# Kernel optimization log

Measured on AMD Instinct MI355X. Metric: run time of the kernel, lower is better.

Reference implementation:

```python
import jax, jax.numpy as jnp
import numpy as np

B, M, S, E, LC, V, HOPS = 16, 2048, 6, 128, 512, 32000, 3
PAD = 1


def setup_inputs() -> dict:
    key = jax.random.key(0)
    ks = jax.random.split(key, 16)
    story = jax.random.randint(ks[0], (B, M, S), 0, V)
    kb_len = jax.random.randint(ks[1], (B,), 0, M - LC)
    conv_len = jax.random.randint(ks[2], (B,), 0, LC)
    hidden = jax.random.normal(ks[3], (1, B, 2 * E), jnp.float32)
    dh_outputs = jax.random.normal(ks[4], (B, LC, E), jnp.float32)
    tf_hidden = jax.random.normal(ks[5], (B, E), jnp.float32)
    query_vector = jax.random.normal(ks[6], (B, E), jnp.float32)
    global_pointer = jax.random.uniform(ks[7], (B, M), jnp.float32)
    C = jax.random.normal(ks[8], (HOPS + 1, V, E), jnp.float32) * 0.1
    C = C.at[:, PAD, :].set(0.0)  # padding_idx row is zero
    s = 0.05
    wA1 = jax.random.normal(ks[9], (2 * E, E), jnp.float32) * s
    bA1 = jnp.zeros((E,), jnp.float32)
    wA2 = jax.random.normal(ks[10], (E, E), jnp.float32) * s
    bA2 = jnp.zeros((E,), jnp.float32)
    wC1 = jax.random.normal(ks[11], (2 * E, E), jnp.float32) * s
    bC1 = jnp.zeros((E,), jnp.float32)
    wC2 = jax.random.normal(ks[12], (E, E), jnp.float32) * s
    bC2 = jnp.zeros((E,), jnp.float32)
    wf = jax.random.normal(ks[13], (2 * E, E), jnp.float32) * s
    bf = jnp.zeros((E,), jnp.float32)
    return dict(story=story, kb_len=kb_len, conv_len=conv_len, hidden=hidden,
                dh_outputs=dh_outputs, tf_hidden=tf_hidden, query_vector=query_vector,
                global_pointer=global_pointer, C=C, wA1=wA1, bA1=bA1, wA2=wA2, bA2=bA2,
                wC1=wC1, bC1=bC1, wC2=wC2, bC2=bC2, wf=wf, bf=bf)


def _lrelu(x):
    return jnp.where(x > 0, x, 0.1 * x)  # LeakyReLU(0.1)


def _mlp(x, w1, b1, w2, b2):
    return _lrelu(x @ w1 + b1) @ w2 + b2


def _add_lm(mem, kb_len, conv_len, dh):
    # mem: [B,M,E]; add dh[bi,:conv_len[bi]] into rows [kb_len, kb_len+conv_len)
    pos = jnp.arange(mem.shape[1])[None, :]            # [1,M]
    idx = pos - kb_len[:, None]                        # [B,M]
    mask = (idx >= 0) & (idx < conv_len[:, None])
    gathered = jnp.take_along_axis(dh, jnp.clip(idx, 0, dh.shape[1] - 1)[..., None], axis=1)
    return mem + jnp.where(mask[..., None], gathered, 0.0)


def reference(story, kb_len, conv_len, hidden, dh_outputs, tf_hidden,
              query_vector, global_pointer, C, wA1, bA1, wA2, bA2,
              wC1, bC1, wC2, bC2, wf, bf):
    # --- load_ent_memory: build m_story_ent (dropout off / eval mode) ---
    u = _lrelu(hidden[0] @ wf + bf)                    # hidden.squeeze(0) -> [B,E]
    tf = jnp.broadcast_to(tf_hidden[:, None, :], (B, M, E))
    m_story = []
    eC = None
    for hop in range(HOPS):
        eA = _add_lm(C[hop][story].sum(2), kb_len, conv_len, dh_outputs)       # [B,M,E]
        eA = _mlp(jnp.concatenate([eA, tf], -1), wA1, bA1, wA2, bA2)
        logit = jnp.einsum('bme,be->bm', eA, u)
        p = jax.nn.softmax(logit, axis=1)
        eC = _add_lm(C[hop + 1][story].sum(2), kb_len, conv_len, dh_outputs)   # [B,M,E]
        eC = _mlp(jnp.concatenate([eC, tf], -1), wC1, bC1, wC2, bC2)
        u = u + jnp.einsum('bme,bm->be', eC, p)
        m_story.append(eA)
    m_story.append(eC)
    # --- forward(query_vector, global_pointer) ---
    uq = query_vector
    gp = global_pointer[..., None]                     # [B,M,1]
    prob_logits = None
    prob_soft = None
    for hop in range(HOPS):
        mA = m_story[hop] * gp
        prob_logits = jnp.einsum('bme,be->bm', mA, uq)
        prob_soft = jax.nn.softmax(prob_logits, axis=1)
        mC = m_story[hop + 1] * gp
        uq = uq + jnp.einsum('bme,bm->be', mC, prob_soft)
    return (prob_soft, prob_logits)
```

## Files before the change

kernel.cpp:

```cpp
#include <hip/hip_runtime.h>
#include <math.h>

#define BB 16
#define MM 2048
#define SS 6
#define EE 128
#define LCC 512
#define VV 32000

typedef __attribute__((ext_vector_type(8))) __bf16 bf16x8;
typedef __attribute__((ext_vector_type(4))) float f32x4;

#define XS_STRIDE 264
#define HS_STRIDE 136

static __device__ inline void cvt8(const float* __restrict__ src, __bf16* __restrict__ dst) {
    const float4 a = *(const float4*)src;
    const float4 b = *(const float4*)(src + 4);
    bf16x8 o;
    o[0] = (__bf16)a.x; o[1] = (__bf16)a.y; o[2] = (__bf16)a.z; o[3] = (__bf16)a.w;
    o[4] = (__bf16)b.x; o[5] = (__bf16)b.y; o[6] = (__bf16)b.z; o[7] = (__bf16)b.w;
    *(bf16x8*)dst = o;
}

#define N_C8  (3 * VV * EE / 8)
#define N_D8  (BB * LCC * EE / 8)
#define N_T8  (BB * EE / 8)
#define N_W1  (256 * 128)
#define N_W2  (128 * 128)
#define N_UQ  (BB * EE)
#define N_PREP (N_C8 + N_D8 + N_T8 + N_W1 + N_W2 + N_UQ)

__global__ __launch_bounds__(256)
void megaprep(const float* __restrict__ C, const float* __restrict__ dh,
              const float* __restrict__ tf, const float* __restrict__ W1,
              const float* __restrict__ W2, const float* __restrict__ query,
              __bf16* __restrict__ Cb, __bf16* __restrict__ dhb,
              __bf16* __restrict__ tfb, __bf16* __restrict__ w1t,
              __bf16* __restrict__ w2t, float* __restrict__ uqA,
              float* __restrict__ uqB)
{
    int i = blockIdx.x * 256 + threadIdx.x;
    if (i < N_C8) { cvt8(C + (size_t)i * 8, Cb + (size_t)i * 8); return; }
    i -= N_C8;
    if (i < N_D8) { cvt8(dh + (size_t)i * 8, dhb + (size_t)i * 8); return; }
    i -= N_D8;
    if (i < N_T8) { cvt8(tf + i * 8, tfb + i * 8); return; }
    i -= N_T8;
    if (i < N_W1) { const int n = i >> 8, k = i & 255; w1t[i] = (__bf16)W1[k * EE + n]; return; }
    i -= N_W1;
    if (i < N_W2) { const int n = i >> 7, k = i & 127; w2t[i] = (__bf16)W2[k * EE + n]; return; }
    i -= N_W2;
    if (i < N_UQ) { uqA[i] = query[i]; uqB[i] = 0.f; }
}

__global__ __launch_bounds__(256)
void embed_mlp_mfma(const int* __restrict__ story,
                    const int* __restrict__ kb_len,
                    const int* __restrict__ conv_len,
                    const __bf16* __restrict__ Cb,
                    const __bf16* __restrict__ dhb,
                    const __bf16* __restrict__ tfb,
                    const __bf16* __restrict__ w1t, const float* __restrict__ b1,
                    const __bf16* __restrict__ w2t, const float* __restrict__ b2,
                    const float* __restrict__ gp, const float* __restrict__ query,
                    __bf16* __restrict__ mout, float* __restrict__ lbuf0)
{
    __shared__ __bf16 Xs[32 * XS_STRIDE];
    __shared__ __bf16 Hs[32 * HS_STRIDE];
    __shared__ int    sidx[32 * SS];
    float* plog = (float*)Hs;

    const int bid  = blockIdx.x;
    const int hop  = bid >> 10;
    const int row0 = (bid & 1023) * 32;
    const int b    = row0 >> 11;
    const int tid  = threadIdx.x;

    const __bf16* Ck = Cb + (size_t)hop * VV * EE;

    for (int i = tid; i < 32 * SS; i += 256) sidx[i] = story[(size_t)row0 * SS + i];

    const int kb   = kb_len[b];
    const int cl   = conv_len[b];
    const int rgrp = tid >> 4;
    const int e8   = (tid & 15) * 8;
    const bf16x8 tf8 = *(const bf16x8*)&tfb[b * EE + e8];
    __syncthreads();

    bf16x8 g[2][SS], dv[2];
    #pragma unroll
    for (int p = 0; p < 2; ++p) {
        const int r = p * 16 + rgrp;
        const int* si = &sidx[r * SS];
        #pragma unroll
        for (int s = 0; s < SS; ++s)
            g[p][s] = *(const bf16x8*)&Ck[(size_t)si[s] * EE + e8];
        const int j = ((row0 + r) & (MM - 1)) - kb;
        if (j >= 0 && j < cl) {
            dv[p] = *(const bf16x8*)&dhb[((size_t)b * LCC + j) * EE + e8];
        } else {
            bf16x8 z;
            #pragma unroll
            for (int q = 0; q < 8; ++q) z[q] = (__bf16)0.f;
            dv[p] = z;
        }
    }
    #pragma unroll
    for (int p = 0; p < 2; ++p) {
        const int r = p * 16 + rgrp;
        bf16x8 pk;
        #pragma unroll
        for (int q = 0; q < 8; ++q) {
            float s = (float)dv[p][q];
            #pragma unroll
            for (int s6 = 0; s6 < SS; ++s6) s += (float)g[p][s6][q];
            pk[q] = (__bf16)s;
        }
        *(bf16x8*)&Xs[r * XS_STRIDE + e8]      = pk;
        *(bf16x8*)&Xs[r * XS_STRIDE + EE + e8] = tf8;
    }
    __syncthreads();

    const int w       = tid >> 6;
    const int lane    = tid & 63;
    const int lr      = lane & 15;
    const int lk      = lane >> 4;
    const int colbase = w * 32;

    f32x4 acc1[2][2];
    #pragma unroll
    for (int i = 0; i < 2; ++i)
        #pragma unroll
        for (int j = 0; j < 2; ++j) acc1[i][j] = (f32x4){0.f, 0.f, 0.f, 0.f};

    for (int ks = 0; ks < 8; ++ks) {
        bf16x8 a[2], bw[2];
        #pragma unroll
        for (int mt = 0; mt < 2; ++mt)
            a[mt] = *(const bf16x8*)&Xs[(mt * 16 + lr) * XS_STRIDE + ks * 32 + lk * 8];
        #pragma unroll
        for (int nt = 0; nt < 2; ++nt)
            bw[nt] = *(const bf16x8*)&w1t[(size_t)(colbase + nt * 16 + lr) * 256 + ks * 32 + lk * 8];
        #pragma unroll
        for (int mt = 0; mt < 2; ++mt)
            #pragma unroll
            for (int nt = 0; nt < 2; ++nt)
                acc1[mt][nt] = __builtin_amdgcn_mfma_f32_16x16x32_bf16(a[mt], bw[nt], acc1[mt][nt], 0, 0, 0);
    }
    {
        const float b1v[2] = { b1[colbase + lr], b1[colbase + 16 + lr] };
        #pragma unroll
        for (int mt = 0; mt < 2; ++mt)
            #pragma unroll
            for (int nt = 0; nt < 2; ++nt)
                #pragma unroll
                for (int reg = 0; reg < 4; ++reg) {
                    float h = acc1[mt][nt][reg] + b1v[nt];
                    h = (h > 0.f) ? h : 0.1f * h;
                    Hs[(mt * 16 + lk * 4 + reg) * HS_STRIDE + colbase + nt * 16 + lr] = (__bf16)h;
                }
    }
    __syncthreads();

    f32x4 acc2[2][2];
    #pragma unroll
    for (int i = 0; i < 2; ++i)
        #pragma unroll
        for (int j = 0; j < 2; ++j) acc2[i][j] = (f32x4){0.f, 0.f, 0.f, 0.f};

    for (int ks = 0; ks < 4; ++ks) {
        bf16x8 a[2], bw[2];
        #pragma unroll
        for (int mt = 0; mt < 2; ++mt)
            a[mt] = *(const bf16x8*)&Hs[(mt * 16 + lr) * HS_STRIDE + ks * 32 + lk * 8];
        #pragma unroll
        for (int nt = 0; nt < 2; ++nt)
            bw[nt] = *(const bf16x8*)&w2t[(size_t)(colbase + nt * 16 + lr) * 128 + ks * 32 + lk * 8];
        #pragma unroll
        for (int mt = 0; mt < 2; ++mt)
            #pragma unroll
            for (int nt = 0; nt < 2; ++nt)
                acc2[mt][nt] = __builtin_amdgcn_mfma_f32_16x16x32_bf16(a[mt], bw[nt], acc2[mt][nt], 0, 0, 0);
    }

    const float b2v[2] = { b2[colbase + lr], b2[colbase + 16 + lr] };

    if (hop == 0) {
        const float qv0 = query[b * EE + colbase + lr];
        const float qv1 = query[b * EE + colbase + 16 + lr];
        __syncthreads();
        #pragma unroll
        for (int mt = 0; mt < 2; ++mt)
            #pragma unroll
            for (int reg = 0; reg < 4; ++reg) {
                float p = (acc2[mt][0][reg] + b2v[0]) * qv0
                        + (acc2[mt][1][reg] + b2v[1]) * qv1;
                p += __shfl_xor(p, 1, 64);
                p += __shfl_xor(p, 2, 64);
                p += __shfl_xor(p, 4, 64);
                p += __shfl_xor(p, 8, 64);
                if (lr == 0) plog[(mt * 16 + lk * 4 + reg) * 4 + w] = p;
            }
        __syncthreads();
        if (tid < 32) {
            const float l = plog[tid * 4] + plog[tid * 4 + 1] + plog[tid * 4 + 2] + plog[tid * 4 + 3];
            lbuf0[row0 + tid] = l * gp[row0 + tid];
        }
    } else {
        __bf16* out = mout + (size_t)(hop - 1) * 32768 * EE;
        #pragma unroll
        for (int mt = 0; mt < 2; ++mt)
            #pragma unroll
            for (int nt = 0; nt < 2; ++nt)
                #pragma unroll
                for (int reg = 0; reg < 4; ++reg) {
                    const int rg_ = row0 + mt * 16 + lk * 4 + reg;
                    out[(size_t)rg_ * EE + colbase + nt * 16 + lr] =
                        (__bf16)(acc2[mt][nt][reg] + b2v[nt]);
                }
    }
}

__global__ __launch_bounds__(256)
void update_kernel(const __bf16* __restrict__ mk, const float* __restrict__ gp,
                   const float* __restrict__ lbuf, float* __restrict__ uq)
{
    __shared__ float redm[4], reds[4];
    __shared__ float wls[64];
    __shared__ float part[4][128];

    const int b      = blockIdx.x >> 5;
    const int rloc0  = (blockIdx.x & 31) * 64;
    const int tid    = threadIdx.x;
    const int lane   = tid & 63;
    const int w      = tid >> 6;
    const float* lb  = lbuf + (size_t)b * MM;

    float v[8];
    float mx = -1e30f;
    #pragma unroll
    for (int i = 0; i < 8; ++i) { v[i] = lb[i * 256 + tid]; mx = fmaxf(mx, v[i]); }
    #pragma unroll
    for (int off = 32; off > 0; off >>= 1) mx = fmaxf(mx, __shfl_xor(mx, off, 64));
    if (lane == 0) redm[w] = mx;
    __syncthreads();
    mx = fmaxf(fmaxf(redm[0], redm[1]), fmaxf(redm[2], redm[3]));
    float sum = 0.f;
    #pragma unroll
    for (int i = 0; i < 8; ++i) sum += __expf(v[i] - mx);
    #pragma unroll
    for (int off = 32; off > 0; off >>= 1) sum += __shfl_xor(sum, off, 64);
    if (lane == 0) reds[w] = sum;
    __syncthreads();
    const float inv = 1.f / (reds[0] + reds[1] + reds[2] + reds[3]);

    if (tid < 64)
        wls[tid] = gp[(size_t)b * MM + rloc0 + tid] * __expf(lb[rloc0 + tid] - mx) * inv;
    __syncthreads();

    const int rgrp = tid >> 4;
    const int e8   = (tid & 15) * 8;
    float acc[8];
    #pragma unroll
    for (int q = 0; q < 8; ++q) acc[q] = 0.f;
    #pragma unroll
    for (int p = 0; p < 4; ++p) {
        const int rl  = p * 16 + rgrp;
        const float wg = wls[rl];
        const bf16x8 vv = *(const bf16x8*)&mk[((size_t)b * MM + rloc0 + rl) * EE + e8];
        #pragma unroll
        for (int q = 0; q < 8; ++q) acc[q] += wg * (float)vv[q];
    }
    #pragma unroll
    for (int q = 0; q < 8; ++q) {
        acc[q] += __shfl_xor(acc[q], 16, 64);
        acc[q] += __shfl_xor(acc[q], 32, 64);
    }
    if (lane < 16) {
        #pragma unroll
        for (int q = 0; q < 8; ++q) part[w][e8 + q] = acc[q];
    }
    __syncthreads();
    if (tid < 128) {
        const float s = part[0][tid] + part[1][tid] + part[2][tid] + part[3][tid];
        atomicAdd(&uq[b * EE + tid], s);
    }
}

__global__ __launch_bounds__(256)
void logits_kernel(const __bf16* __restrict__ mk, const float* __restrict__ gp,
                   const float* __restrict__ uqa, const float* __restrict__ uqb,
                   float* __restrict__ out)
{
    __shared__ float uqs[128];
    const int row0 = blockIdx.x * 64;
    const int b    = row0 >> 11;
    const int tid  = threadIdx.x;
    if (tid < 128) uqs[tid] = uqa[b * EE + tid] + (uqb ? uqb[b * EE + tid] : 0.f);
    __syncthreads();
    const int w = tid >> 6, lane = tid & 63;
    const int g = lane >> 4, l16 = lane & 15;
    float u[8];
    #pragma unroll
    for (int j = 0; j < 8; ++j) u[j] = uqs[l16 * 8 + j];
    #pragma unroll
    for (int it = 0; it < 4; ++it) {
        const int row = row0 + it * 16 + w * 4 + g;
        const bf16x8 v = *(const bf16x8*)&mk[(size_t)row * EE + l16 * 8];
        float p = 0.f;
        #pragma unroll
        for (int j = 0; j < 8; ++j) p += (float)v[j] * u[j];
        p += __shfl_xor(p, 1, 64);
        p += __shfl_xor(p, 2, 64);
        p += __shfl_xor(p, 4, 64);
        p += __shfl_xor(p, 8, 64);
        if (l16 == 0) out[row] = p * gp[row];
    }
}

__global__ __launch_bounds__(256)
void softmax_final(const float* __restrict__ logits, float* __restrict__ soft)
{
    __shared__ float redm[4], reds[4];
    const int b = blockIdx.x, tid = threadIdx.x;
    const int lane = tid & 63, w = tid >> 6;
    const float* lb = logits + (size_t)b * MM;
    float v[8];
    float mx = -1e30f;
    #pragma unroll
    for (int i = 0; i < 8; ++i) { v[i] = lb[i * 256 + tid]; mx = fmaxf(mx, v[i]); }
    #pragma unroll
    for (int off = 32; off > 0; off >>= 1) mx = fmaxf(mx, __shfl_xor(mx, off, 64));
    if (lane == 0) redm[w] = mx;
    __syncthreads();
    mx = fmaxf(fmaxf(redm[0], redm[1]), fmaxf(redm[2], redm[3]));
    float sum = 0.f;
    #pragma unroll
    for (int i = 0; i < 8; ++i) { v[i] = __expf(v[i] - mx); sum += v[i]; }
    #pragma unroll
    for (int off = 32; off > 0; off >>= 1) sum += __shfl_xor(sum, off, 64);
    if (lane == 0) reds[w] = sum;
    __syncthreads();
    const float inv = 1.f / (reds[0] + reds[1] + reds[2] + reds[3]);
    #pragma unroll
    for (int i = 0; i < 8; ++i) soft[(size_t)b * MM + i * 256 + tid] = v[i] * inv;
}

extern "C" void kernel_launch(void* const* d_in, const int* in_sizes, int n_in,
                              void* d_out, int out_size, void* d_ws, size_t ws_size,
                              hipStream_t stream) {
    const int*   story    = (const int*)d_in[0];
    const int*   kb_len   = (const int*)d_in[1];
    const int*   conv_len = (const int*)d_in[2];
    const float* dh       = (const float*)d_in[4];
    const float* tf       = (const float*)d_in[5];
    const float* query    = (const float*)d_in[6];
    const float* gp       = (const float*)d_in[7];
    const float* C        = (const float*)d_in[8];
    const float* wA1      = (const float*)d_in[9];
    const float* bA1      = (const float*)d_in[10];
    const float* wA2      = (const float*)d_in[11];
    const float* bA2      = (const float*)d_in[12];

    char* ws = (char*)d_ws;
    const size_t M_ELEMS = (size_t)32768 * EE;
    size_t off = 0;
    __bf16* m   = (__bf16*)(ws + off); off += 2 * M_ELEMS * sizeof(__bf16);
    __bf16* Cb  = (__bf16*)(ws + off); off += (size_t)3 * VV * EE * sizeof(__bf16);
    __bf16* dhb = (__bf16*)(ws + off); off += (size_t)BB * LCC * EE * sizeof(__bf16);
    __bf16* tfb = (__bf16*)(ws + off); off += (size_t)BB * EE * sizeof(__bf16);
    __bf16* w1t = (__bf16*)(ws + off); off += 256 * 128 * sizeof(__bf16);
    __bf16* w2t = (__bf16*)(ws + off); off += 128 * 128 * sizeof(__bf16);
    float* lbuf = (float*)(ws + off);  off += (size_t)BB * MM * sizeof(float);
    float* uqA  = (float*)(ws + off);  off += (size_t)BB * EE * sizeof(float);
    float* uqB  = (float*)(ws + off);  off += (size_t)BB * EE * sizeof(float);

    float* out_soft   = (float*)d_out;
    float* out_logits = out_soft + (size_t)BB * MM;

    megaprep<<<N_PREP / 256, 256, 0, stream>>>(C, dh, tf, wA1, wA2, query,
                                               Cb, dhb, tfb, w1t, w2t, uqA, uqB);
    embed_mlp_mfma<<<3072, 256, 0, stream>>>(story, kb_len, conv_len, Cb, dhb, tfb,
                                             w1t, bA1, w2t, bA2, gp, query, m, lbuf);
    update_kernel<<<512, 256, 0, stream>>>(m, gp, lbuf, uqA);
    logits_kernel<<<512, 256, 0, stream>>>(m, gp, uqA, nullptr, lbuf);
    update_kernel<<<512, 256, 0, stream>>>(m + M_ELEMS, gp, lbuf, uqB);
    logits_kernel<<<512, 256, 0, stream>>>(m + M_ELEMS, gp, uqA, uqB, out_logits);
    softmax_final<<<BB, 256, 0, stream>>>(out_logits, out_soft);
}
```

Baseline: 195.1 us.

## Fuse hop update, logits and softmax into one per-batch tail kernel

Replaces the five tail launches (two update, two logits, one softmax) with a single kernel that runs one 1024-thread block per batch and loops over the hops, keeping uq and the logits in shared memory. This removes the atomics, the uq initialisation in the prep kernel and several launch gaps. The trade-off is that only 16 blocks run the tail, so most CUs sit idle while each block streams 2 MB of bf16 per hop. Separately, the embed kernel now reuses the Xs shared buffer for Hs, with an extra barrier before Hs is written, and declares launch bounds of 8 blocks per CU to raise occupancy.

```diff
diff --git a/kernel.cpp b/kernel.cpp
--- a/kernel.cpp
+++ b/kernel.cpp
@@ -28,17 +28,15 @@
 #define N_T8  (BB * EE / 8)
 #define N_W1  (256 * 128)
 #define N_W2  (128 * 128)
-#define N_UQ  (BB * EE)
-#define N_PREP (N_C8 + N_D8 + N_T8 + N_W1 + N_W2 + N_UQ)
+#define N_PREP (N_C8 + N_D8 + N_T8 + N_W1 + N_W2)
 
 __global__ __launch_bounds__(256)
 void megaprep(const float* __restrict__ C, const float* __restrict__ dh,
               const float* __restrict__ tf, const float* __restrict__ W1,
-              const float* __restrict__ W2, const float* __restrict__ query,
+              const float* __restrict__ W2,
               __bf16* __restrict__ Cb, __bf16* __restrict__ dhb,
               __bf16* __restrict__ tfb, __bf16* __restrict__ w1t,
-              __bf16* __restrict__ w2t, float* __restrict__ uqA,
-              float* __restrict__ uqB)
+              __bf16* __restrict__ w2t)
 {
     int i = blockIdx.x * 256 + threadIdx.x;
     if (i < N_C8) { cvt8(C + (size_t)i * 8, Cb + (size_t)i * 8); return; }
@@ -49,12 +47,10 @@
     i -= N_T8;
     if (i < N_W1) { const int n = i >> 8, k = i & 255; w1t[i] = (__bf16)W1[k * EE + n]; return; }
     i -= N_W1;
-    if (i < N_W2) { const int n = i >> 7, k = i & 127; w2t[i] = (__bf16)W2[k * EE + n]; return; }
-    i -= N_W2;
-    if (i < N_UQ) { uqA[i] = query[i]; uqB[i] = 0.f; }
-}
-
-__global__ __launch_bounds__(256)
+    if (i < N_W2) { const int n = i >> 7, k = i & 127; w2t[i] = (__bf16)W2[k * EE + n]; }
+}
+
+__global__ __launch_bounds__(256, 8)
 void embed_mlp_mfma(const int* __restrict__ story,
                     const int* __restrict__ kb_len,
                     const int* __restrict__ conv_len,
@@ -67,9 +63,9 @@
                     __bf16* __restrict__ mout, float* __restrict__ lbuf0)
 {
     __shared__ __bf16 Xs[32 * XS_STRIDE];
-    __shared__ __bf16 Hs[32 * HS_STRIDE];
     __shared__ int    sidx[32 * SS];
-    float* plog = (float*)Hs;
+    __bf16* Hs   = Xs;
+    float*  plog = (float*)Xs;
 
     const int bid  = blockIdx.x;
     const int hop  = bid >> 10;
@@ -148,6 +144,7 @@
             for (int nt = 0; nt < 2; ++nt)
                 acc1[mt][nt] = __builtin_amdgcn_mfma_f32_16x16x32_bf16(a[mt], bw[nt], acc1[mt][nt], 0, 0, 0);
     }
+    __syncthreads();
     {
         const float b1v[2] = { b1[colbase + lr], b1[colbase + 16 + lr] };
         #pragma unroll
@@ -222,129 +219,111 @@
     }
 }
 
-__global__ __launch_bounds__(256)
-void update_kernel(const __bf16* __restrict__ mk, const float* __restrict__ gp,
-                   const float* __restrict__ lbuf, float* __restrict__ uq)
-{
-    __shared__ float redm[4], reds[4];
-    __shared__ float wls[64];
-    __shared__ float part[4][128];
-
-    const int b      = blockIdx.x >> 5;
-    const int rloc0  = (blockIdx.x & 31) * 64;
-    const int tid    = threadIdx.x;
-    const int lane   = tid & 63;
-    const int w      = tid >> 6;
-    const float* lb  = lbuf + (size_t)b * MM;
-
-    float v[8];
-    float mx = -1e30f;
-    #pragma unroll
-    for (int i = 0; i < 8; ++i) { v[i] = lb[i * 256 + tid]; mx = fmaxf(mx, v[i]); }
-    #pragma unroll
-    for (int off = 32; off > 0; off >>= 1) mx = fmaxf(mx, __shfl_xor(mx, off, 64));
-    if (lane == 0) redm[w] = mx;
-    __syncthreads();
-    mx = fmaxf(fmaxf(redm[0], redm[1]), fmaxf(redm[2], redm[3]));
-    float sum = 0.f;
-    #pragma unroll
-    for (int i = 0; i < 8; ++i) sum += __expf(v[i] - mx);
-    #pragma unroll
-    for (int off = 32; off > 0; off >>= 1) sum += __shfl_xor(sum, off, 64);
-    if (lane == 0) reds[w] = sum;
-    __syncthreads();
-    const float inv = 1.f / (reds[0] + reds[1] + reds[2] + reds[3]);
-
-    if (tid < 64)
-        wls[tid] = gp[(size_t)b * MM + rloc0 + tid] * __expf(lb[rloc0 + tid] - mx) * inv;
-    __syncthreads();
-
-    const int rgrp = tid >> 4;
-    const int e8   = (tid & 15) * 8;
-    float acc[8];
-    #pragma unroll
-    for (int q = 0; q < 8; ++q) acc[q] = 0.f;
-    #pragma unroll
-    for (int p = 0; p < 4; ++p) {
-        const int rl  = p * 16 + rgrp;
-        const float wg = wls[rl];
-        const bf16x8 vv = *(const bf16x8*)&mk[((size_t)b * MM + rloc0 + rl) * EE + e8];
-        #pragma unroll
-        for (int q = 0; q < 8; ++q) acc[q] += wg * (float)vv[q];
-    }
-    #pragma unroll
-    for (int q = 0; q < 8; ++q) {
-        acc[q] += __shfl_xor(acc[q], 16, 64);
-        acc[q] += __shfl_xor(acc[q], 32, 64);
-    }
-    if (lane < 16) {
-        #pragma unroll
-        for (int q = 0; q < 8; ++q) part[w][e8 + q] = acc[q];
-    }
-    __syncthreads();
-    if (tid < 128) {
-        const float s = part[0][tid] + part[1][tid] + part[2][tid] + part[3][tid];
-        atomicAdd(&uq[b * EE + tid], s);
-    }
-}
-
-__global__ __launch_bounds__(256)
-void logits_kernel(const __bf16* __restrict__ mk, const float* __restrict__ gp,
-                   const float* __restrict__ uqa, const float* __restrict__ uqb,
-                   float* __restrict__ out)
+__global__ __launch_bounds__(1024)
+void tail_kernel(const __bf16* __restrict__ m, const float* __restrict__ gp,
+                 const float* __restrict__ lbuf0, const float* __restrict__ query,
+                 float* __restrict__ out_logits, float* __restrict__ out_soft)
 {
     __shared__ float uqs[128];
-    const int row0 = blockIdx.x * 64;
-    const int b    = row0 >> 11;
+    __shared__ float wls[2048];
+    __shared__ float lls[2048];
+    __shared__ float part[16][128];
+    __shared__ float redm[16], reds[16];
+
+    const int b    = blockIdx.x;
     const int tid  = threadIdx.x;
-    if (tid < 128) uqs[tid] = uqa[b * EE + tid] + (uqb ? uqb[b * EE + tid] : 0.f);
-    __syncthreads();
-    const int w = tid >> 6, lane = tid & 63;
-    const int g = lane >> 4, l16 = lane & 15;
-    float u[8];
-    #pragma unroll
-    for (int j = 0; j < 8; ++j) u[j] = uqs[l16 * 8 + j];
-    #pragma unroll
-    for (int it = 0; it < 4; ++it) {
-        const int row = row0 + it * 16 + w * 4 + g;
-        const bf16x8 v = *(const bf16x8*)&mk[(size_t)row * EE + l16 * 8];
-        float p = 0.f;
-        #pragma unroll
-        for (int j = 0; j < 8; ++j) p += (float)v[j] * u[j];
-        p += __shfl_xor(p, 1, 64);
-        p += __shfl_xor(p, 2, 64);
-        p += __shfl_xor(p, 4, 64);
-        p += __shfl_xor(p, 8, 64);
-        if (l16 == 0) out[row] = p * gp[row];
-    }
-}
-
-__global__ __launch_bounds__(256)
-void softmax_final(const float* __restrict__ logits, float* __restrict__ soft)
-{
-    __shared__ float redm[4], reds[4];
-    const int b = blockIdx.x, tid = threadIdx.x;
-    const int lane = tid & 63, w = tid >> 6;
-    const float* lb = logits + (size_t)b * MM;
-    float v[8];
-    float mx = -1e30f;
-    #pragma unroll
-    for (int i = 0; i < 8; ++i) { v[i] = lb[i * 256 + tid]; mx = fmaxf(mx, v[i]); }
-    #pragma unroll
-    for (int off = 32; off > 0; off >>= 1) mx = fmaxf(mx, __shfl_xor(mx, off, 64));
-    if (lane == 0) redm[w] = mx;
-    __syncthreads();
-    mx = fmaxf(fmaxf(redm[0], redm[1]), fmaxf(redm[2], redm[3]));
-    float sum = 0.f;
-    #pragma unroll
-    for (int i = 0; i < 8; ++i) { v[i] = __expf(v[i] - mx); sum += v[i]; }
-    #pragma unroll
-    for (int off = 32; off > 0; off >>= 1) sum += __shfl_xor(sum, off, 64);
-    if (lane == 0) reds[w] = sum;
-    __syncthreads();
-    const float inv = 1.f / (reds[0] + reds[1] + reds[2] + reds[3]);
-    #pragma unroll
-    for (int i = 0; i < 8; ++i) soft[(size_t)b * MM + i * 256 + tid] = v[i] * inv;
+    const int w    = tid >> 6;
+    const int lane = tid & 63;
+    const int g    = lane >> 4;
+    const int l16  = lane & 15;
+    const float* gpb = gp + (size_t)b * MM;
+
+    if (tid < 128) uqs[tid] = query[b * EE + tid];
+    lls[tid]        = lbuf0[(size_t)b * MM + tid];
+    lls[tid + 1024] = lbuf0[(size_t)b * MM + tid + 1024];
+    __syncthreads();
+
+    for (int hop = 0; hop < 3; ++hop) {
+        const float v0 = lls[tid], v1 = lls[tid + 1024];
+        float mx = fmaxf(v0, v1);
+        #pragma unroll
+        for (int off = 32; off > 0; off >>= 1) mx = fmaxf(mx, __shfl_xor(mx, off, 64));
+        if (lane == 0) redm[w] = mx;
+        __syncthreads();
+        float bmx = redm[0];
+        #pragma unroll
+        for (int i = 1; i < 16; ++i) bmx = fmaxf(bmx, redm[i]);
+        const float e0 = __expf(v0 - bmx), e1 = __expf(v1 - bmx);
+        float sm = e0 + e1;
+        #pragma unroll
+        for (int off = 32; off > 0; off >>= 1) sm += __shfl_xor(sm, off, 64);
+        if (lane == 0) reds[w] = sm;
+        __syncthreads();
+        float bs = 0.f;
+        #pragma unroll
+        for (int i = 0; i < 16; ++i) bs += reds[i];
+        const float inv = 1.f / bs;
+
+        if (hop == 2) {
+            out_soft[(size_t)b * MM + tid]        = e0 * inv;
+            out_soft[(size_t)b * MM + tid + 1024] = e1 * inv;
+            return;
+        }
+        wls[tid]        = e0 * inv * gpb[tid];
+        wls[tid + 1024] = e1 * inv * gpb[tid + 1024];
+        __syncthreads();
+
+        const __bf16* mh = m + ((size_t)hop * 32768 + (size_t)b * MM) * EE;
+
+        float acc[8];
+        #pragma unroll
+        for (int q = 0; q < 8; ++q) acc[q] = 0.f;
+        for (int it = 0; it < 32; ++it) {
+            const int row = w * 128 + it * 4 + g;
+            const bf16x8 mv = *(const bf16x8*)&mh[(size_t)row * EE + l16 * 8];
+            const float wg = wls[row];
+            #pragma unroll
+            for (int q = 0; q < 8; ++q) acc[q] += wg * (float)mv[q];
+        }
+        #pragma unroll
+        for (int q = 0; q < 8; ++q) {
+            acc[q] += __shfl_xor(acc[q], 16, 64);
+            acc[q] += __shfl_xor(acc[q], 32, 64);
+        }
+        if (lane < 16) {
+            #pragma unroll
+            for (int q = 0; q < 8; ++q) part[w][l16 * 8 + q] = acc[q];
+        }
+        __syncthreads();
+        if (tid < 128) {
+            float s = uqs[tid];
+            #pragma unroll
+            for (int ww = 0; ww < 16; ++ww) s += part[ww][tid];
+            uqs[tid] = s;
+        }
+        __syncthreads();
+
+        float u[8];
+        #pragma unroll
+        for (int j = 0; j < 8; ++j) u[j] = uqs[l16 * 8 + j];
+        for (int it = 0; it < 32; ++it) {
+            const int row = w * 128 + it * 4 + g;
+            const bf16x8 mv = *(const bf16x8*)&mh[(size_t)row * EE + l16 * 8];
+            float p = 0.f;
+            #pragma unroll
+            for (int j = 0; j < 8; ++j) p += (float)mv[j] * u[j];
+            p += __shfl_xor(p, 1, 64);
+            p += __shfl_xor(p, 2, 64);
+            p += __shfl_xor(p, 4, 64);
+            p += __shfl_xor(p, 8, 64);
+            if (l16 == 0) {
+                const float lv = p * gpb[row];
+                lls[row] = lv;
+                if (hop == 1) out_logits[(size_t)b * MM + row] = lv;
+            }
+        }
+        __syncthreads();
+    }
 }
 
 extern "C" void kernel_launch(void* const* d_in, const int* in_sizes, int n_in,
@@ -373,19 +352,13 @@
     __bf16* w1t = (__bf16*)(ws + off); off += 256 * 128 * sizeof(__bf16);
     __bf16* w2t = (__bf16*)(ws + off); off += 128 * 128 * sizeof(__bf16);
     float* lbuf = (float*)(ws + off);  off += (size_t)BB * MM * sizeof(float);
-    float* uqA  = (float*)(ws + off);  off += (size_t)BB * EE * sizeof(float);
-    float* uqB  = (float*)(ws + off);  off += (size_t)BB * EE * sizeof(float);
 
     float* out_soft   = (float*)d_out;
     float* out_logits = out_soft + (size_t)BB * MM;
 
-    megaprep<<<N_PREP / 256, 256, 0, stream>>>(C, dh, tf, wA1, wA2, query,
-                                               Cb, dhb, tfb, w1t, w2t, uqA, uqB);
+    megaprep<<<N_PREP / 256, 256, 0, stream>>>(C, dh, tf, wA1, wA2,
+                                               Cb, dhb, tfb, w1t, w2t);
     embed_mlp_mfma<<<3072, 256, 0, stream>>>(story, kb_len, conv_len, Cb, dhb, tfb,
                                              w1t, bA1, w2t, bA2, gp, query, m, lbuf);
-    update_kernel<<<512, 256, 0, stream>>>(m, gp, lbuf, uqA);
-    logits_kernel<<<512, 256, 0, stream>>>(m, gp, uqA, nullptr, lbuf);
-    update_kernel<<<512, 256, 0, stream>>>(m + M_ELEMS, gp, lbuf, uqB);
-    logits_kernel<<<512, 256, 0, stream>>>(m + M_ELEMS, gp, uqA, uqB, out_logits);
-    softmax_final<<<BB, 256, 0, stream>>>(out_logits, out_soft);
-}
+    tail_kernel<<<BB, 1024, 0, stream>>>(m, gp, lbuf, query, out_logits, out_soft);
+}
```

Measured after the change: 239.2 us. 22.6% more time.

## Gather fp32 embeddings directly instead of pre-converting the whole table to bf16

Applied to the files above, without the earlier changes.

Removes the prep pass that converted the full embedding tables, dialogue outputs and tf vector to bf16. The embed kernel now gathers fp32 rows, sums them in fp32 and packs to bf16 in shared memory. The query term is folded into the logits kernel instead of being copied into the accumulator. This trades a large streaming conversion pass for twice the bytes per gathered row.

```diff
diff --git a/kernel.cpp b/kernel.cpp
--- a/kernel.cpp
+++ b/kernel.cpp
@@ -14,53 +14,38 @@
 #define XS_STRIDE 264
 #define HS_STRIDE 136
 
-static __device__ inline void cvt8(const float* __restrict__ src, __bf16* __restrict__ dst) {
-    const float4 a = *(const float4*)src;
-    const float4 b = *(const float4*)(src + 4);
-    bf16x8 o;
-    o[0] = (__bf16)a.x; o[1] = (__bf16)a.y; o[2] = (__bf16)a.z; o[3] = (__bf16)a.w;
-    o[4] = (__bf16)b.x; o[5] = (__bf16)b.y; o[6] = (__bf16)b.z; o[7] = (__bf16)b.w;
-    *(bf16x8*)dst = o;
-}
-
-#define N_C8  (3 * VV * EE / 8)
-#define N_D8  (BB * LCC * EE / 8)
-#define N_T8  (BB * EE / 8)
+static __device__ inline unsigned short bfbits(float x) {
+    __bf16 h = (__bf16)x;
+    return __builtin_bit_cast(unsigned short, h);
+}
+
 #define N_W1  (256 * 128)
 #define N_W2  (128 * 128)
 #define N_UQ  (BB * EE)
-#define N_PREP (N_C8 + N_D8 + N_T8 + N_W1 + N_W2 + N_UQ)
-
-__global__ __launch_bounds__(256)
-void megaprep(const float* __restrict__ C, const float* __restrict__ dh,
-              const float* __restrict__ tf, const float* __restrict__ W1,
-              const float* __restrict__ W2, const float* __restrict__ query,
-              __bf16* __restrict__ Cb, __bf16* __restrict__ dhb,
-              __bf16* __restrict__ tfb, __bf16* __restrict__ w1t,
-              __bf16* __restrict__ w2t, float* __restrict__ uqA,
-              float* __restrict__ uqB)
+#define N_PREP (N_W1 + N_W2 + 2 * N_UQ)
+
+__global__ __launch_bounds__(256)
+void prep_small(const float* __restrict__ W1, const float* __restrict__ W2,
+                __bf16* __restrict__ w1t, __bf16* __restrict__ w2t,
+                float* __restrict__ uqA, float* __restrict__ uqB)
 {
     int i = blockIdx.x * 256 + threadIdx.x;
-    if (i < N_C8) { cvt8(C + (size_t)i * 8, Cb + (size_t)i * 8); return; }
-    i -= N_C8;
-    if (i < N_D8) { cvt8(dh + (size_t)i * 8, dhb + (size_t)i * 8); return; }
-    i -= N_D8;
-    if (i < N_T8) { cvt8(tf + i * 8, tfb + i * 8); return; }
-    i -= N_T8;
     if (i < N_W1) { const int n = i >> 8, k = i & 255; w1t[i] = (__bf16)W1[k * EE + n]; return; }
     i -= N_W1;
     if (i < N_W2) { const int n = i >> 7, k = i & 127; w2t[i] = (__bf16)W2[k * EE + n]; return; }
     i -= N_W2;
-    if (i < N_UQ) { uqA[i] = query[i]; uqB[i] = 0.f; }
+    if (i < N_UQ) { uqA[i] = 0.f; return; }
+    i -= N_UQ;
+    if (i < N_UQ) { uqB[i] = 0.f; }
 }
 
 __global__ __launch_bounds__(256)
 void embed_mlp_mfma(const int* __restrict__ story,
                     const int* __restrict__ kb_len,
                     const int* __restrict__ conv_len,
-                    const __bf16* __restrict__ Cb,
-                    const __bf16* __restrict__ dhb,
-                    const __bf16* __restrict__ tfb,
+                    const float* __restrict__ dh,
+                    const float* __restrict__ tf,
+                    const float* __restrict__ C,
                     const __bf16* __restrict__ w1t, const float* __restrict__ b1,
                     const __bf16* __restrict__ w2t, const float* __restrict__ b2,
                     const float* __restrict__ gp, const float* __restrict__ query,
@@ -77,48 +62,38 @@
     const int b    = row0 >> 11;
     const int tid  = threadIdx.x;
 
-    const __bf16* Ck = Cb + (size_t)hop * VV * EE;
+    const float* Ck = C + (size_t)hop * VV * EE;
 
     for (int i = tid; i < 32 * SS; i += 256) sidx[i] = story[(size_t)row0 * SS + i];
 
     const int kb   = kb_len[b];
     const int cl   = conv_len[b];
-    const int rgrp = tid >> 4;
-    const int e8   = (tid & 15) * 8;
-    const bf16x8 tf8 = *(const bf16x8*)&tfb[b * EE + e8];
-    __syncthreads();
-
-    bf16x8 g[2][SS], dv[2];
-    #pragma unroll
-    for (int p = 0; p < 2; ++p) {
-        const int r = p * 16 + rgrp;
+    const int rgrp = tid >> 5;
+    const int e4   = (tid & 31) * 4;
+    const float4 tf4 = *(const float4*)&tf[b * EE + e4];
+    ushort4 tfp;
+    tfp.x = bfbits(tf4.x); tfp.y = bfbits(tf4.y); tfp.z = bfbits(tf4.z); tfp.w = bfbits(tf4.w);
+    __syncthreads();
+
+    for (int chunk = 0; chunk < 4; ++chunk) {
+        const int r  = chunk * 8 + rgrp;
         const int* si = &sidx[r * SS];
+        float4 v[SS];
         #pragma unroll
         for (int s = 0; s < SS; ++s)
-            g[p][s] = *(const bf16x8*)&Ck[(size_t)si[s] * EE + e8];
+            v[s] = *(const float4*)&Ck[(size_t)si[s] * EE + e4];
         const int j = ((row0 + r) & (MM - 1)) - kb;
-        if (j >= 0 && j < cl) {
-            dv[p] = *(const bf16x8*)&dhb[((size_t)b * LCC + j) * EE + e8];
-        } else {
-            bf16x8 z;
-            #pragma unroll
-            for (int q = 0; q < 8; ++q) z[q] = (__bf16)0.f;
-            dv[p] = z;
+        float4 acc = {0.f, 0.f, 0.f, 0.f};
+        if (j >= 0 && j < cl)
+            acc = *(const float4*)&dh[((size_t)b * LCC + j) * EE + e4];
+        #pragma unroll
+        for (int s = 0; s < SS; ++s) {
+            acc.x += v[s].x; acc.y += v[s].y; acc.z += v[s].z; acc.w += v[s].w;
         }
-    }
-    #pragma unroll
-    for (int p = 0; p < 2; ++p) {
-        const int r = p * 16 + rgrp;
-        bf16x8 pk;
-        #pragma unroll
-        for (int q = 0; q < 8; ++q) {
-            float s = (float)dv[p][q];
-            #pragma unroll
-            for (int s6 = 0; s6 < SS; ++s6) s += (float)g[p][s6][q];
-            pk[q] = (__bf16)s;
-        }
-        *(bf16x8*)&Xs[r * XS_STRIDE + e8]      = pk;
-        *(bf16x8*)&Xs[r * XS_STRIDE + EE + e8] = tf8;
+        ushort4 pk;
+        pk.x = bfbits(acc.x); pk.y = bfbits(acc.y); pk.z = bfbits(acc.z); pk.w = bfbits(acc.w);
+        *(ushort4*)&Xs[r * XS_STRIDE + e4]      = pk;
+        *(ushort4*)&Xs[r * XS_STRIDE + EE + e4] = tfp;
     }
     __syncthreads();
 
@@ -290,14 +265,16 @@
 
 __global__ __launch_bounds__(256)
 void logits_kernel(const __bf16* __restrict__ mk, const float* __restrict__ gp,
-                   const float* __restrict__ uqa, const float* __restrict__ uqb,
-                   float* __restrict__ out)
+                   const float* __restrict__ query, const float* __restrict__ uqa,
+                   const float* __restrict__ uqb, float* __restrict__ out)
 {
     __shared__ float uqs[128];
     const int row0 = blockIdx.x * 64;
     const int b    = row0 >> 11;
     const int tid  = threadIdx.x;
-    if (tid < 128) uqs[tid] = uqa[b * EE + tid] + (uqb ? uqb[b * EE + tid] : 0.f);
+    if (tid < 128)
+        uqs[tid] = query[b * EE + tid] + uqa[b * EE + tid]
+                 + (uqb ? uqb[b * EE + tid] : 0.f);
     __syncthreads();
     const int w = tid >> 6, lane = tid & 63;
     const int g = lane >> 4, l16 = lane & 15;
@@ -367,9 +344,6 @@
     const size_t M_ELEMS = (size_t)32768 * EE;
     size_t off = 0;
     __bf16* m   = (__bf16*)(ws + off); off += 2 * M_ELEMS * sizeof(__bf16);
-    __bf16* Cb  = (__bf16*)(ws + off); off += (size_t)3 * VV * EE * sizeof(__bf16);
-    __bf16* dhb = (__bf16*)(ws + off); off += (size_t)BB * LCC * EE * sizeof(__bf16);
-    __bf16* tfb = (__bf16*)(ws + off); off += (size_t)BB * EE * sizeof(__bf16);
     __bf16* w1t = (__bf16*)(ws + off); off += 256 * 128 * sizeof(__bf16);
     __bf16* w2t = (__bf16*)(ws + off); off += 128 * 128 * sizeof(__bf16);
     float* lbuf = (float*)(ws + off);  off += (size_t)BB * MM * sizeof(float);
@@ -379,13 +353,12 @@
     float* out_soft   = (float*)d_out;
     float* out_logits = out_soft + (size_t)BB * MM;
 
-    megaprep<<<N_PREP / 256, 256, 0, stream>>>(C, dh, tf, wA1, wA2, query,
-                                               Cb, dhb, tfb, w1t, w2t, uqA, uqB);
-    embed_mlp_mfma<<<3072, 256, 0, stream>>>(story, kb_len, conv_len, Cb, dhb, tfb,
+    prep_small<<<N_PREP / 256, 256, 0, stream>>>(wA1, wA2, w1t, w2t, uqA, uqB);
+    embed_mlp_mfma<<<3072, 256, 0, stream>>>(story, kb_len, conv_len, dh, tf, C,
                                              w1t, bA1, w2t, bA2, gp, query, m, lbuf);
     update_kernel<<<512, 256, 0, stream>>>(m, gp, lbuf, uqA);
-    logits_kernel<<<512, 256, 0, stream>>>(m, gp, uqA, nullptr, lbuf);
+    logits_kernel<<<512, 256, 0, stream>>>(m, gp, query, uqA, nullptr, lbuf);
     update_kernel<<<512, 256, 0, stream>>>(m + M_ELEMS, gp, lbuf, uqB);
-    logits_kernel<<<512, 256, 0, stream>>>(m + M_ELEMS, gp, uqA, uqB, out_logits);
+    logits_kernel<<<512, 256, 0, stream>>>(m + M_ELEMS, gp, query, uqA, uqB, out_logits);
     softmax_final<<<BB, 256, 0, stream>>>(out_logits, out_soft);
 }
```

Result: no change. 197.7 us (+1.3%).
